# Performance work log

Hardware: AMD Instinct MI355X
Metric: run time of the kernel (lower is better)

## Reference

```python
import jax, jax.numpy as jnp
import numpy as np


def _lstm_step(h, c, x, W, U, b):
    # Keras gate order: i, f, g(candidate), o
    z = x @ W + h @ U + b  # [B, 4H]
    i, f, g, o = jnp.split(z, 4, axis=-1)
    i = jax.nn.sigmoid(i)
    f = jax.nn.sigmoid(f)
    g = jnp.tanh(g)
    o = jax.nn.sigmoid(o)
    c_new = f * c + i * g
    h_new = o * jnp.tanh(c_new)
    return h_new, c_new


def setup_inputs() -> dict:
    key = jax.random.key(0)
    ks = jax.random.split(key, 8)
    B, T, F, H = 2048, 512, 8, 128
    s = lambda k, shape, scale: (jax.random.normal(k, shape, jnp.float32) * scale)
    return {
        "x": jax.random.normal(ks[0], (B, T, F), jnp.float32),
        "W_enc": s(ks[1], (F, 4 * H), 0.1),
        "U_enc": s(ks[2], (H, 4 * H), 0.1),
        "b_enc": jnp.zeros((4 * H,), jnp.float32),
        "W_dec": s(ks[3], (F, 4 * H), 0.1),
        "U_dec": s(ks[4], (H, 4 * H), 0.1),
        "b_dec": jnp.zeros((4 * H,), jnp.float32),
        "W_out": s(ks[5], (H, F), 0.1),
        "b_out": jnp.zeros((F,), jnp.float32),
    }


def reference(x, W_enc, U_enc, b_enc, W_dec, U_dec, b_dec, W_out, b_out):
    B, T, F = x.shape
    H = U_enc.shape[0]
    h0 = jnp.zeros((B, H), x.dtype)
    c0 = jnp.zeros((B, H), x.dtype)

    # Encoder LSTM: only the final (h, c) state is consumed downstream.
    def enc_step(carry, xt):
        h, c = carry
        h, c = _lstm_step(h, c, xt, W_enc, U_enc, b_enc)
        return (h, c), None

    (h_enc, c_enc), _ = jax.lax.scan(enc_step, (h0, c0), jnp.swapaxes(x, 0, 1))

    def dec_step(carry, _):
        y, h, c = carry
        h, c = _lstm_step(h, c, y, W_dec, U_dec, b_dec)
        y = jax.nn.relu(h @ W_out + b_out)
        return (y, h, c), y

    _, ys = jax.lax.scan(dec_step, (x[:, -1, :], h_enc, c_enc), None, length=T)
    return jnp.swapaxes(ys, 0, 1)  # [B, T, F]
```

## Files before the change

### kernel.cpp

```cpp
#include <hip/hip_runtime.h>


namespace {

typedef __attribute__((ext_vector_type(8))) short bf16x8;
typedef __attribute__((ext_vector_type(4))) float f32x4;
typedef __attribute__((ext_vector_type(2))) unsigned int uint2v;
typedef __attribute__((ext_vector_type(4))) unsigned int uint4v;
typedef __attribute__((ext_vector_type(2))) unsigned short ushort2v;
typedef __attribute__((ext_vector_type(2))) float float2v;

constexpr int T = 512, F = 8, H = 128, G4 = 512, NTH = 512;
constexpr int HS = 136;
constexpr int XS = 40;
constexpr int CS = 16;

struct __align__(16) Smem {
  unsigned short hb[2][16][HS];
  unsigned short xp[2][16][XS];
  unsigned short xq[2][CS][16][XS];
};

__device__ __forceinline__ float rcpf(float v) { return __builtin_amdgcn_rcpf(v); }
__device__ __forceinline__ float sigm(float v) { return rcpf(1.0f + __expf(-v)); }
__device__ __forceinline__ float tanh_(float v) { return 1.0f - 2.0f * rcpf(__expf(2.0f * v) + 1.0f); }

__device__ __forceinline__ unsigned short bf_rtn(float v) {
  unsigned u = __float_as_uint(v);
  return (unsigned short)((u + 0x7FFFu + ((u >> 16) & 1u)) >> 16);
}
__device__ __forceinline__ void split_tr(float v, unsigned short& hi, unsigned short& lo) {
  unsigned u = __float_as_uint(v);
  hi = (unsigned short)(u >> 16);
  lo = bf_rtn(v - __uint_as_float(u & 0xFFFF0000u));
}

__device__ __forceinline__ float pair_fold(float a, float b) {
  uint2v r = __builtin_amdgcn_permlane32_swap(__float_as_uint(a), __float_as_uint(b), false, false);
  return __uint_as_float(r[0]) + __uint_as_float(r[1]);
}

__device__ __forceinline__ void bar_lgkm() {
  __asm__ __volatile__("s_waitcnt lgkmcnt(0)" ::: "memory");
  __builtin_amdgcn_s_barrier();
  __asm__ __volatile__("" ::: "memory");
}

__global__ __launch_bounds__(NTH, 2)
void rae_v8(const float* __restrict__ x,
            const float* __restrict__ Wenc, const float* __restrict__ Uenc, const float* __restrict__ benc,
            const float* __restrict__ Wdec, const float* __restrict__ Udec, const float* __restrict__ bdec,
            const float* __restrict__ Wout, const float* __restrict__ boutg,
            float* __restrict__ out)
{
  __shared__ Smem s;
  const int tid = threadIdx.x, lane = tid & 63, w = tid >> 6;
  const int q = lane >> 4, n = lane & 15;
  const long gb = (long)blockIdx.x * 8;

  {
    uint4v z4 = {0u, 0u, 0u, 0u};
#pragma unroll 4
    for (int i = tid; i < (int)(sizeof(Smem) / 16); i += NTH)
      ((uint4v*)&s)[i] = z4;
  }
  __syncthreads();

  const int sfp = tid & 3, srow = (tid >> 2) & 7, sts = tid >> 5;
  const long xsb = (gb + srow) * (long)(T * F) + sts * F + sfp * 2;

  {
    float2v xv0 = *(const float2v*)&x[xsb];
    unsigned short h0s, l0s, h1s, l1s;
    split_tr(xv0[0], h0s, l0s); split_tr(xv0[1], h1s, l1s);
    ushort2v hh = {h0s, h1s}, ll = {l0s, l1s};
    *(ushort2v*)&s.xq[0][sts][srow][sfp * 2] = hh;
    *(ushort2v*)&s.xq[0][sts][srow + 8][sfp * 2] = ll;
    *(ushort2v*)&s.xq[0][sts][srow + 8][8 + sfp * 2] = hh;
  }

  bf16x8 Bw[4];
#pragma unroll
  for (int kt = 0; kt < 4; ++kt) {
    bf16x8 bw;
#pragma unroll
    for (int j = 0; j < 8; ++j) {
      unsigned short hv, lv; split_tr(Wout[(kt * 32 + q * 8 + j) * F + (n & 7)], hv, lv);
      bw[j] = (short)((n < 8) ? hv : lv);
    }
    Bw[kt] = bw;
  }
  const float boutr = boutg[n & 7];
  float cst[2] = {0.f, 0.f};
  __syncthreads();

  const float probe = pair_fold(0.0f, 1.0f);
  const int r0 = ((lane & 31) >> 4) * 4 + (int)probe;
  const int cc = w * 16 + n;

  bf16x8 A[4], Ax;
  {
    bf16x8 zz = {0, 0, 0, 0, 0, 0, 0, 0};
#pragma unroll
    for (int kt = 0; kt < 4; ++kt) A[kt] = zz;
    Ax = zz;
  }

  bf16x8 B1[5][4];
  f32x4 bias4[4];
  const f32x4 zero4 = {0.f, 0.f, 0.f, 0.f};

  auto preload = [&](const float* U, const float* W, const float* bi) {
#pragma unroll
    for (int kt = 0; kt < 5; ++kt)
#pragma unroll
      for (int g = 0; g < 4; ++g) {
        const int col = g * 128 + w * 16 + n;
        bf16x8 b1;
#pragma unroll
        for (int j = 0; j < 8; ++j) {
          unsigned short v = 0;
          if (kt < 4) {
            v = bf_rtn(U[(kt * 32 + q * 8 + j) * G4 + col]);
          } else {
            const int kk = q * 8 + j;
            unsigned short hv, lv;
            if (kk < 8)       { split_tr(W[kk * G4 + col], hv, lv); v = hv; }
            else if (kk < 16) { split_tr(W[(kk - 8) * G4 + col], hv, lv); v = lv; }
          }
          b1[j] = (short)v;
        }
        B1[kt][g] = b1;
      }
#pragma unroll
    for (int g = 0; g < 4; ++g) {
      const float b = 0.5f * bi[g * 128 + w * 16 + n];
      bias4[g] = f32x4{b, b, b, b};
    }
  };

  auto activ_store = [&](f32x4 (&acc)[4], int slot) {
    float zA[4], zB[4];
#pragma unroll
    for (int g = 0; g < 4; ++g) {
      zA[g] = pair_fold(acc[g][0], acc[g][2]);
      zB[g] = pair_fold(acc[g][1], acc[g][3]);
    }
    cst[0] = sigm(zA[1]) * cst[0] + sigm(zA[0]) * tanh_(zA[2]);
    cst[1] = sigm(zB[1]) * cst[1] + sigm(zB[0]) * tanh_(zB[2]);
    const float h0 = sigm(zA[3]) * tanh_(cst[0]);
    const float h1 = sigm(zB[3]) * tanh_(cst[1]);
    unsigned short hv0, lv0, hv1, lv1;
    split_tr(h0, hv0, lv0); split_tr(h1, hv1, lv1);
    s.hb[slot][r0][cc]     = hv0;  s.hb[slot][r0 + 8][cc] = lv0;
    s.hb[slot][r0 + 1][cc] = hv1;  s.hb[slot][r0 + 9][cc] = lv1;
  };

  preload(Uenc, Wenc, benc);

  Ax = *(const bf16x8*)&s.xq[0][0][n][q * 8];

  float2v xv = {0.f, 0.f};

#pragma unroll 2
  for (int t = 0; t < T; ++t) {
    const int pnxt = (t & 1) ^ 1;
    const bool do_load  = (((t + 2) & (CS - 1)) == 0) && (t + 2 < T);
    const bool do_write = (((t + 1) & (CS - 1)) == 0) && (t + 1 < T);
    if (do_load) xv = *(const float2v*)&x[xsb + (long)(t + 2) * F];

    f32x4 acc[4];
#pragma unroll
    for (int g = 0; g < 4; ++g)
      acc[g] = __builtin_amdgcn_mfma_f32_16x16x32_bf16(Ax, B1[4][g], bias4[g], 0, 0, 0);
#pragma unroll
    for (int kt = 0; kt < 4; ++kt)
#pragma unroll
      for (int g = 0; g < 4; ++g)
        acc[g] = __builtin_amdgcn_mfma_f32_16x16x32_bf16(A[kt], B1[kt][g], acc[g], 0, 0, 0);

    activ_store(acc, pnxt);

    if (do_write) {
      const int cb = ((t + 1) >> 4) & 1;
      unsigned short h0s, l0s, h1s, l1s;
      split_tr(xv[0], h0s, l0s); split_tr(xv[1], h1s, l1s);
      ushort2v hh = {h0s, h1s}, ll = {l0s, l1s};
      *(ushort2v*)&s.xq[cb][sts][srow][sfp * 2] = hh;
      *(ushort2v*)&s.xq[cb][sts][srow + 8][sfp * 2] = ll;
      *(ushort2v*)&s.xq[cb][sts][srow + 8][8 + sfp * 2] = hh;
    }

    bar_lgkm();

    const int tn = t + 1;
    Ax = *(const bf16x8*)&s.xq[(tn >> 4) & 1][tn & (CS - 1)][n][q * 8];
#pragma unroll
    for (int kt = 0; kt < 4; ++kt)
      A[kt] = *(const bf16x8*)&s.hb[pnxt][n][kt * 32 + q * 8];
  }

  preload(Udec, Wdec, bdec);

  if (tid < 64) {
    unsigned short hv, lv;
    split_tr(x[(gb + (tid >> 3)) * (long)(T * F) + (T - 1) * F + (tid & 7)], hv, lv);
    s.xp[1][tid >> 3][tid & 7] = hv;
    s.xp[1][(tid >> 3) + 8][tid & 7] = lv;
    s.xp[1][(tid >> 3) + 8][(tid & 7) + 8] = hv;
  }
  __syncthreads();

  f32x4 hacc[4];
#pragma unroll
  for (int g = 0; g < 4; ++g)
    hacc[g] = __builtin_amdgcn_mfma_f32_16x16x32_bf16(A[0], B1[0][g], bias4[g], 0, 0, 0);
#pragma unroll
  for (int kt = 1; kt < 4; ++kt)
#pragma unroll
    for (int g = 0; g < 4; ++g)
      hacc[g] = __builtin_amdgcn_mfma_f32_16x16x32_bf16(A[kt], B1[kt][g], hacc[g], 0, 0, 0);
  Ax = *(const bf16x8*)&s.xp[1][n][q * 8];

  float* o0 = out + ((gb + r0) * (long)T) * F + n;
  float* o1 = o0 + (long)T * F;

#pragma unroll 2
  for (int t = 0; t < T; ++t) {
    const int wA = (t & 1) ^ 1;

    f32x4 acc[4];
#pragma unroll
    for (int g = 0; g < 4; ++g)
      acc[g] = __builtin_amdgcn_mfma_f32_16x16x32_bf16(Ax, B1[4][g], hacc[g], 0, 0, 0);

    activ_store(acc, wA);

    bar_lgkm();

#pragma unroll
    for (int kt = 0; kt < 4; ++kt)
      A[kt] = *(const bf16x8*)&s.hb[wA][n][kt * 32 + q * 8];

    f32x4 ay = __builtin_amdgcn_mfma_f32_16x16x32_bf16(A[0], Bw[0], zero4, 0, 0, 0);
#pragma unroll
    for (int kt = 1; kt < 4; ++kt)
      ay = __builtin_amdgcn_mfma_f32_16x16x32_bf16(A[kt], Bw[kt], ay, 0, 0, 0);

#pragma unroll
    for (int g = 0; g < 4; ++g)
      hacc[g] = __builtin_amdgcn_mfma_f32_16x16x32_bf16(A[0], B1[0][g], bias4[g], 0, 0, 0);
#pragma unroll
    for (int kt = 1; kt < 4; ++kt)
#pragma unroll
      for (int g = 0; g < 4; ++g)
        hacc[g] = __builtin_amdgcn_mfma_f32_16x16x32_bf16(A[kt], B1[kt][g], hacc[g], 0, 0, 0);

    const float sA = pair_fold(ay[0], ay[2]);
    const float sB = pair_fold(ay[1], ay[3]);
    const float y0 = fmaxf(sA + __shfl_xor(sA, 8, 64) + boutr, 0.f);
    const float y1 = fmaxf(sB + __shfl_xor(sB, 8, 64) + boutr, 0.f);
    if (n < 8) {
      if (w == 0) { o0[t * F] = y0; o1[t * F] = y1; }
      unsigned short hv, lv;
      split_tr(y0, hv, lv);
      s.xp[t & 1][r0][n]         = hv;
      s.xp[t & 1][r0 + 8][n]     = lv;
      s.xp[t & 1][r0 + 8][n + 8] = hv;
      split_tr(y1, hv, lv);
      s.xp[t & 1][r0 + 1][n]     = hv;
      s.xp[t & 1][r0 + 9][n]     = lv;
      s.xp[t & 1][r0 + 9][n + 8] = hv;
    }
    Ax = *(const bf16x8*)&s.xp[t & 1][n][q * 8];
  }
}

}

extern "C" void kernel_launch(void* const* d_in, const int* in_sizes, int n_in,
                              void* d_out, int out_size, void* d_ws, size_t ws_size,
                              hipStream_t stream) {
  const float* x    = (const float*)d_in[0];
  const float* Wenc = (const float*)d_in[1];
  const float* Uenc = (const float*)d_in[2];
  const float* benc = (const float*)d_in[3];
  const float* Wdec = (const float*)d_in[4];
  const float* Udec = (const float*)d_in[5];
  const float* bdec = (const float*)d_in[6];
  const float* Wout = (const float*)d_in[7];
  const float* bout = (const float*)d_in[8];
  float* out = (float*)d_out;

  const int Bsz = in_sizes[0] / (T * F);
  const int nblocks = Bsz / 8;
  rae_v8<<<dim3(nblocks), dim3(NTH), 0, stream>>>(
      x, Wenc, Uenc, benc, Wdec, Udec, bdec, Wout, bout, out);
}
```

Before: 992.6 us.

## Fold log2e into LSTM weights, interleave gate MFMAs with activations, add setprio

Pre-scales the gate weights and biases by log2(e) so the sigmoid and tanh can call the hardware v_exp_f32 (base-2 exp) directly, without a multiply per call. The candidate-gate tanh output carries the same scale, so the cell state stays consistent in scaled units. The gate matmuls are now computed one gate at a time, and each finished gate's activation is placed between the MFMA chains of the next gates to hide transcendental latency on the serial timestep path. s_setprio is raised around the MFMA bursts, and the activation math is written in packed float2 form. It relies on inline asm and on the compiler keeping the interleaved order, and rounding differs slightly because the weights are pre-scaled before bf16 conversion.

```diff
diff --git a/kernel.cpp b/kernel.cpp
--- a/kernel.cpp
+++ b/kernel.cpp
@@ -14,6 +14,7 @@
 constexpr int HS = 136;
 constexpr int XS = 40;
 constexpr int CS = 16;
+constexpr float L2E = 1.4426950408889634f;
 
 struct __align__(16) Smem {
   unsigned short hb[2][16][HS];
@@ -22,8 +23,9 @@
 };
 
 __device__ __forceinline__ float rcpf(float v) { return __builtin_amdgcn_rcpf(v); }
-__device__ __forceinline__ float sigm(float v) { return rcpf(1.0f + __expf(-v)); }
-__device__ __forceinline__ float tanh_(float v) { return 1.0f - 2.0f * rcpf(__expf(2.0f * v) + 1.0f); }
+
+__device__ __forceinline__ float exp2p(float x) { float r; asm("v_exp_f32 %0, %1" : "=v"(r) : "v"(x)); return r; }
+__device__ __forceinline__ float exp2m(float x) { float r; asm("v_exp_f32_e64 %0, -%1" : "=v"(r) : "v"(x)); return r; }
 
 __device__ __forceinline__ unsigned short bf_rtn(float v) {
   unsigned u = __float_as_uint(v);
@@ -35,9 +37,27 @@
   lo = bf_rtn(v - __uint_as_float(u & 0xFFFF0000u));
 }
 
+__device__ __forceinline__ float2v sigm2(float2v z) {
+  float2v d = { exp2m(z[0]) + 1.f, exp2m(z[1]) + 1.f };
+  return (float2v){ rcpf(d[0]), rcpf(d[1]) };
+}
+__device__ __forceinline__ float2v gtanh2(float2v z) {
+  float2v zz = z + z;
+  float2v d = { exp2p(zz[0]) + 1.f, exp2p(zz[1]) + 1.f };
+  return (float2v){ fmaf(rcpf(d[0]), -2.f * L2E, L2E), fmaf(rcpf(d[1]), -2.f * L2E, L2E) };
+}
+__device__ __forceinline__ float2v ttanh2(float2v c) {
+  float2v cc = c + c;
+  float2v d = { exp2p(cc[0]) + 1.f, exp2p(cc[1]) + 1.f };
+  return (float2v){ fmaf(rcpf(d[0]), -2.f, 1.f), fmaf(rcpf(d[1]), -2.f, 1.f) };
+}
+
 __device__ __forceinline__ float pair_fold(float a, float b) {
   uint2v r = __builtin_amdgcn_permlane32_swap(__float_as_uint(a), __float_as_uint(b), false, false);
   return __uint_as_float(r[0]) + __uint_as_float(r[1]);
+}
+__device__ __forceinline__ float2v fold4(const f32x4& z4) {
+  return (float2v){ pair_fold(z4[0], z4[2]), pair_fold(z4[1], z4[3]) };
 }
 
 __device__ __forceinline__ void bar_lgkm() {
@@ -47,11 +67,11 @@
 }
 
 __global__ __launch_bounds__(NTH, 2)
-void rae_v8(const float* __restrict__ x,
-            const float* __restrict__ Wenc, const float* __restrict__ Uenc, const float* __restrict__ benc,
-            const float* __restrict__ Wdec, const float* __restrict__ Udec, const float* __restrict__ bdec,
-            const float* __restrict__ Wout, const float* __restrict__ boutg,
-            float* __restrict__ out)
+void rae_v10(const float* __restrict__ x,
+             const float* __restrict__ Wenc, const float* __restrict__ Uenc, const float* __restrict__ benc,
+             const float* __restrict__ Wdec, const float* __restrict__ Udec, const float* __restrict__ bdec,
+             const float* __restrict__ Wout, const float* __restrict__ boutg,
+             float* __restrict__ out)
 {
   __shared__ Smem s;
   const int tid = threadIdx.x, lane = tid & 63, w = tid >> 6;
@@ -91,7 +111,7 @@
     Bw[kt] = bw;
   }
   const float boutr = boutg[n & 7];
-  float cst[2] = {0.f, 0.f};
+  float2v cst2 = {0.f, 0.f};
   __syncthreads();
 
   const float probe = pair_fold(0.0f, 1.0f);
@@ -121,12 +141,12 @@
         for (int j = 0; j < 8; ++j) {
           unsigned short v = 0;
           if (kt < 4) {
-            v = bf_rtn(U[(kt * 32 + q * 8 + j) * G4 + col]);
+            v = bf_rtn(L2E * U[(kt * 32 + q * 8 + j) * G4 + col]);
           } else {
             const int kk = q * 8 + j;
             unsigned short hv, lv;
-            if (kk < 8)       { split_tr(W[kk * G4 + col], hv, lv); v = hv; }
-            else if (kk < 16) { split_tr(W[(kk - 8) * G4 + col], hv, lv); v = lv; }
+            if (kk < 8)       { split_tr(L2E * W[kk * G4 + col], hv, lv); v = hv; }
+            else if (kk < 16) { split_tr(L2E * W[(kk - 8) * G4 + col], hv, lv); v = lv; }
           }
           b1[j] = (short)v;
         }
@@ -134,24 +154,16 @@
       }
 #pragma unroll
     for (int g = 0; g < 4; ++g) {
-      const float b = 0.5f * bi[g * 128 + w * 16 + n];
+      const float b = 0.5f * L2E * bi[g * 128 + w * 16 + n];
       bias4[g] = f32x4{b, b, b, b};
     }
   };
 
-  auto activ_store = [&](f32x4 (&acc)[4], int slot) {
-    float zA[4], zB[4];
-#pragma unroll
-    for (int g = 0; g < 4; ++g) {
-      zA[g] = pair_fold(acc[g][0], acc[g][2]);
-      zB[g] = pair_fold(acc[g][1], acc[g][3]);
-    }
-    cst[0] = sigm(zA[1]) * cst[0] + sigm(zA[0]) * tanh_(zA[2]);
-    cst[1] = sigm(zB[1]) * cst[1] + sigm(zB[0]) * tanh_(zB[2]);
-    const float h0 = sigm(zA[3]) * tanh_(cst[0]);
-    const float h1 = sigm(zB[3]) * tanh_(cst[1]);
+  auto finish_store = [&](float2v sf, float2v si, float2v gg, float2v zo, int slot) {
+    cst2 = sf * cst2 + si * gg;
+    const float2v hh = sigm2(zo) * ttanh2(cst2);
     unsigned short hv0, lv0, hv1, lv1;
-    split_tr(h0, hv0, lv0); split_tr(h1, hv1, lv1);
+    split_tr(hh[0], hv0, lv0); split_tr(hh[1], hv1, lv1);
     s.hb[slot][r0][cc]     = hv0;  s.hb[slot][r0 + 8][cc] = lv0;
     s.hb[slot][r0 + 1][cc] = hv1;  s.hb[slot][r0 + 9][cc] = lv1;
   };
@@ -169,17 +181,30 @@
     const bool do_write = (((t + 1) & (CS - 1)) == 0) && (t + 1 < T);
     if (do_load) xv = *(const float2v*)&x[xsb + (long)(t + 2) * F];
 
-    f32x4 acc[4];
-#pragma unroll
-    for (int g = 0; g < 4; ++g)
-      acc[g] = __builtin_amdgcn_mfma_f32_16x16x32_bf16(Ax, B1[4][g], bias4[g], 0, 0, 0);
-#pragma unroll
-    for (int kt = 0; kt < 4; ++kt)
-#pragma unroll
-      for (int g = 0; g < 4; ++g)
-        acc[g] = __builtin_amdgcn_mfma_f32_16x16x32_bf16(A[kt], B1[kt][g], acc[g], 0, 0, 0);
-
-    activ_store(acc, pnxt);
+    f32x4 zf4, zi4, zg4, zo4;
+    __builtin_amdgcn_s_setprio(1);
+    zf4 = __builtin_amdgcn_mfma_f32_16x16x32_bf16(Ax, B1[4][1], bias4[1], 0, 0, 0);
+#pragma unroll
+    for (int kt = 0; kt < 4; ++kt)
+      zf4 = __builtin_amdgcn_mfma_f32_16x16x32_bf16(A[kt], B1[kt][1], zf4, 0, 0, 0);
+    zi4 = __builtin_amdgcn_mfma_f32_16x16x32_bf16(Ax, B1[4][0], bias4[0], 0, 0, 0);
+#pragma unroll
+    for (int kt = 0; kt < 4; ++kt)
+      zi4 = __builtin_amdgcn_mfma_f32_16x16x32_bf16(A[kt], B1[kt][0], zi4, 0, 0, 0);
+    const float2v sf = sigm2(fold4(zf4));
+    zg4 = __builtin_amdgcn_mfma_f32_16x16x32_bf16(Ax, B1[4][2], bias4[2], 0, 0, 0);
+#pragma unroll
+    for (int kt = 0; kt < 4; ++kt)
+      zg4 = __builtin_amdgcn_mfma_f32_16x16x32_bf16(A[kt], B1[kt][2], zg4, 0, 0, 0);
+    const float2v si = sigm2(fold4(zi4));
+    zo4 = __builtin_amdgcn_mfma_f32_16x16x32_bf16(Ax, B1[4][3], bias4[3], 0, 0, 0);
+#pragma unroll
+    for (int kt = 0; kt < 4; ++kt)
+      zo4 = __builtin_amdgcn_mfma_f32_16x16x32_bf16(A[kt], B1[kt][3], zo4, 0, 0, 0);
+    __builtin_amdgcn_s_setprio(0);
+    const float2v gg = gtanh2(fold4(zg4));
+
+    finish_store(sf, si, gg, fold4(zo4), pnxt);
 
     if (do_write) {
       const int cb = ((t + 1) >> 4) & 1;
@@ -229,12 +254,15 @@
   for (int t = 0; t < T; ++t) {
     const int wA = (t & 1) ^ 1;
 
-    f32x4 acc[4];
-#pragma unroll
-    for (int g = 0; g < 4; ++g)
-      acc[g] = __builtin_amdgcn_mfma_f32_16x16x32_bf16(Ax, B1[4][g], hacc[g], 0, 0, 0);
-
-    activ_store(acc, wA);
+    f32x4 zf4 = __builtin_amdgcn_mfma_f32_16x16x32_bf16(Ax, B1[4][1], hacc[1], 0, 0, 0);
+    f32x4 zi4 = __builtin_amdgcn_mfma_f32_16x16x32_bf16(Ax, B1[4][0], hacc[0], 0, 0, 0);
+    const float2v sf = sigm2(fold4(zf4));
+    f32x4 zg4 = __builtin_amdgcn_mfma_f32_16x16x32_bf16(Ax, B1[4][2], hacc[2], 0, 0, 0);
+    const float2v si = sigm2(fold4(zi4));
+    f32x4 zo4 = __builtin_amdgcn_mfma_f32_16x16x32_bf16(Ax, B1[4][3], hacc[3], 0, 0, 0);
+    const float2v gg = gtanh2(fold4(zg4));
+
+    finish_store(sf, si, gg, fold4(zo4), wA);
 
     bar_lgkm();
 
@@ -242,6 +270,7 @@
     for (int kt = 0; kt < 4; ++kt)
       A[kt] = *(const bf16x8*)&s.hb[wA][n][kt * 32 + q * 8];
 
+    __builtin_amdgcn_s_setprio(1);
     f32x4 ay = __builtin_amdgcn_mfma_f32_16x16x32_bf16(A[0], Bw[0], zero4, 0, 0, 0);
 #pragma unroll
     for (int kt = 1; kt < 4; ++kt)
@@ -255,11 +284,12 @@
 #pragma unroll
       for (int g = 0; g < 4; ++g)
         hacc[g] = __builtin_amdgcn_mfma_f32_16x16x32_bf16(A[kt], B1[kt][g], hacc[g], 0, 0, 0);
-
-    const float sA = pair_fold(ay[0], ay[2]);
-    const float sB = pair_fold(ay[1], ay[3]);
-    const float y0 = fmaxf(sA + __shfl_xor(sA, 8, 64) + boutr, 0.f);
-    const float y1 = fmaxf(sB + __shfl_xor(sB, 8, 64) + boutr, 0.f);
+    __builtin_amdgcn_s_setprio(0);
+
+    const float2v sy = { pair_fold(ay[0], ay[2]), pair_fold(ay[1], ay[3]) };
+    const float2v so = { __shfl_xor(sy[0], 8, 64), __shfl_xor(sy[1], 8, 64) };
+    const float2v yraw = sy + so + (float2v){boutr, boutr};
+    const float y0 = fmaxf(yraw[0], 0.f), y1 = fmaxf(yraw[1], 0.f);
     if (n < 8) {
       if (w == 0) { o0[t * F] = y0; o1[t * F] = y1; }
       unsigned short hv, lv;
@@ -294,6 +324,6 @@
 
   const int Bsz = in_sizes[0] / (T * F);
   const int nblocks = Bsz / 8;
-  rae_v8<<<dim3(nblocks), dim3(NTH), 0, stream>>>(
+  rae_v10<<<dim3(nblocks), dim3(NTH), 0, stream>>>(
       x, Wenc, Uenc, benc, Wdec, Udec, bdec, Wout, bout, out);
 }
```

Measured after the change: 990.7 us. About the same (-0.2%).
